# Kernel tuning notes

Measured on AMD Instinct MI355X. Metric: run time of the kernel, lower is better.

## Reference

```python
import jax, jax.numpy as jnp
import numpy as np

EPS = 1e-7

def _dubbed_squash(v):
    norm = jnp.linalg.norm(v, axis=-1, keepdims=True)
    coef = 1.0 - 1.0 / (jnp.exp(norm) + EPS)
    return coef * v / (norm + EPS)

def setup_inputs() -> dict:
    key = jax.random.key(0)
    k1, k2, k3 = jax.random.split(key, 3)
    B, N, dp = 16, 1152, 8   # batch, num_primary_caps, dim_primary_caps
    D, dd = 10, 16           # num_digit_caps, dim_digit_caps
    primary_caps = jax.random.normal(k1, (B, N, dp), dtype=jnp.float32)
    W = jax.random.normal(k2, (D, N, dd, dp), dtype=jnp.float32) * 0.05
    B_prior = jax.random.normal(k3, (D, 1, N), dtype=jnp.float32) * 0.05
    return {"primary_caps": primary_caps, "W": W, "B_prior": B_prior}

def reference(primary_caps, W, B_prior):
    dp = primary_caps.shape[-1]
    # votes: U_hat[b,d,n,j] = W[d,n,j,i] @ u[b,n,i]   (replaces the tf.map_fn)
    U_hat = jnp.einsum('dnji,bni->bdnj', W, primary_caps)  # [B,D,N,dd]
    # self-similarity score matrix (as in original: full NxN matmul)
    A = jnp.einsum('bdnj,bdmj->bdnm', U_hat, U_hat) / jnp.sqrt(
        jnp.asarray(dp, dtype=primary_caps.dtype))          # [B,D,N,N]
    A_sum = jnp.sum(A, axis=2, keepdims=True)               # [B,D,1,N]
    C = jax.nn.softmax(A_sum, axis=1)                       # softmax over digit axis
    # weighted combine with learned log-priors: (B+C) @ U_hat -> [B,D,1,dd] -> squeeze
    S = jnp.einsum('bdkn,bdnj->bdj', B_prior[None] + C, U_hat)  # [B,D,dd]
    return _dubbed_squash(S)
```

## Files before the change

kernel.cpp:

```cpp
#include <hip/hip_runtime.h>

constexpr int BN = 16, NN = 1152, DP = 8, ND = 10, DD = 16;
constexpr int NBLK = BN * ND;
constexpr int GG = 64;
constexpr int KPT = NN / GG;
constexpr unsigned MAG1 = 0xC0FFEE01u;
constexpr int SPIN_CAP = 1 << 20;

__device__ __forceinline__ float ld_dev(const float* p) {
    return __hip_atomic_load(p, __ATOMIC_RELAXED, __HIP_MEMORY_SCOPE_AGENT);
}
__device__ __forceinline__ void st_dev(float* p, float v) {
    __hip_atomic_store(p, v, __ATOMIC_RELAXED, __HIP_MEMORY_SCOPE_AGENT);
}

__global__ __launch_bounds__(1024) void caps_one(
    const float* __restrict__ u, const float* __restrict__ W,
    const float* __restrict__ Bp, float* __restrict__ A,
    unsigned* __restrict__ flags, float* __restrict__ out)
{
    __shared__ float ul[NN * DP];
    __shared__ float coeff[NN];
    __shared__ float Tpart[GG][17];
    __shared__ float Tl[16];
    __shared__ float Spart[GG][17];

    const int t = threadIdx.x;
    const int x = blockIdx.x;
    const int i = (x & 7) * 20 + (x >> 3);
    const int b = i & 15, d = i >> 4;
    const int j = t & 15, g = t >> 4;
    constexpr float RS8 = 0.35355339059327373f;

    {
        const float4* src = reinterpret_cast<const float4*>(u + (size_t)b * NN * DP);
        float4* dst4 = reinterpret_cast<float4*>(ul);
        for (int i2 = t; i2 < NN * DP / 4; i2 += 1024) dst4[i2] = src[i2];
    }
    __syncthreads();

    float uh[KPT];
    float tacc = 0.f;
    const float* Wd = W + (size_t)d * NN * DD * DP;
#pragma unroll 6
    for (int k = 0; k < KPT; ++k) {
        const int n = g + GG * k;
        const float4 w0 = *reinterpret_cast<const float4*>(
            Wd + ((size_t)n * DD + j) * DP);
        const float4 w1 = *reinterpret_cast<const float4*>(
            Wd + ((size_t)n * DD + j) * DP + 4);
        const float4 u0 = reinterpret_cast<const float4*>(ul)[n * 2];
        const float4 u1 = reinterpret_cast<const float4*>(ul)[n * 2 + 1];
        const float s = w0.x * u0.x + w0.y * u0.y + w0.z * u0.z + w0.w * u0.w
                      + w1.x * u1.x + w1.y * u1.y + w1.z * u1.z + w1.w * u1.w;
        uh[k] = s;
        tacc += s;
    }

    Tpart[g][j] = tacc;
    __syncthreads();
    if (t < 16) {
        float s = 0.f;
#pragma unroll
        for (int gg = 0; gg < GG; ++gg) s += Tpart[gg][t];
        Tl[t] = s;
    }
    __syncthreads();

    {
        float* Arow = A + (size_t)(b * ND + d) * NN;
        const float Tj = Tl[j];
#pragma unroll
        for (int k = 0; k < KPT; ++k) {
            float v = Tj * uh[k];
            v += __shfl_xor(v, 8, 16);
            v += __shfl_xor(v, 4, 16);
            v += __shfl_xor(v, 2, 16);
            v += __shfl_xor(v, 1, 16);
            if (j == 0) st_dev(Arow + (g + GG * k), v * RS8);
        }
    }

    __syncthreads();
    if (t == 0)
        __hip_atomic_store(&flags[b * ND + d], MAG1, __ATOMIC_RELAXED,
                           __HIP_MEMORY_SCOPE_AGENT);
    if (t < ND) {
        int spins = 0;
        while (__hip_atomic_load(&flags[b * ND + t], __ATOMIC_RELAXED,
                                 __HIP_MEMORY_SCOPE_AGENT) != MAG1) {
            __builtin_amdgcn_s_sleep(2);
            if (++spins > SPIN_CAP) break;
        }
    }
    asm volatile("" ::: "memory");
    __syncthreads();

    {
        const float* Ab = A + (size_t)b * ND * NN;
        for (int n = t; n < NN; n += 1024) {
            float aq[ND];
#pragma unroll
            for (int q = 0; q < ND; ++q) aq[q] = ld_dev(Ab + (size_t)q * NN + n);
            float m = aq[0];
#pragma unroll
            for (int q = 1; q < ND; ++q) m = fmaxf(m, aq[q]);
            float se = 0.f;
#pragma unroll
            for (int q = 0; q < ND; ++q) { aq[q] = expf(aq[q] - m); se += aq[q]; }
            coeff[n] = Bp[(size_t)d * NN + n] + aq[d] / se;
        }
    }
    __syncthreads();

    float sacc = 0.f;
#pragma unroll
    for (int k = 0; k < KPT; ++k) sacc += coeff[g + GG * k] * uh[k];
    Spart[g][j] = sacc;
    __syncthreads();
    if (t < 16) {
        float Sv = 0.f;
#pragma unroll
        for (int gg = 0; gg < GG; ++gg) Sv += Spart[gg][t];
        float n2 = Sv * Sv;
#pragma unroll
        for (int off = 8; off >= 1; off >>= 1) n2 += __shfl_xor(n2, off, 16);
        const float nrm = sqrtf(n2);
        const float coef = 1.f - 1.f / (expf(nrm) + 1e-7f);
        out[((size_t)b * ND + d) * DD + t] = Sv * (coef / (nrm + 1e-7f));
    }
}

extern "C" void kernel_launch(void* const* d_in, const int* in_sizes, int n_in,
                              void* d_out, int out_size, void* d_ws, size_t ws_size,
                              hipStream_t stream) {
    const float* u  = nullptr;
    const float* W  = nullptr;
    const float* Bp = nullptr;
    for (int i = 0; i < n_in; ++i) {
        const int s = in_sizes[i];
        if (s == BN * NN * DP)            u  = (const float*)d_in[i];
        else if (s == ND * NN * DD * DP)  W  = (const float*)d_in[i];
        else if (s == ND * NN)            Bp = (const float*)d_in[i];
    }
    float* out = (float*)d_out;
    char*  wsc = (char*)d_ws;
    float*    A     = (float*)wsc;
    unsigned* flags = (unsigned*)(wsc + (1u << 20));

    caps_one<<<dim3(NBLK), 1024, 0, stream>>>(u, W, Bp, A, flags, out);
}
```

Baseline: 76.43 us.

## Replace per-element atomic A accesses with plain ops plus explicit cache writeback/invalidate

Drops the relaxed agent-scope atomic loads and stores on the score array A and uses plain stores and float2 vector loads instead. Cross-block visibility is kept by issuing an L2 writeback before the flag store and a cache invalidate after spinning on the flags. It also prefetches the B_prior row into shared memory at the start, overlapping it with the u load. The risk is memory-ordering correctness: the invalidate runs only in the polling threads before the barrier, and the inline asm cache instructions are specific to this architecture.

```diff
diff --git a/kernel.cpp b/kernel.cpp
--- a/kernel.cpp
+++ b/kernel.cpp
@@ -7,19 +7,13 @@
 constexpr unsigned MAG1 = 0xC0FFEE01u;
 constexpr int SPIN_CAP = 1 << 20;
 
-__device__ __forceinline__ float ld_dev(const float* p) {
-    return __hip_atomic_load(p, __ATOMIC_RELAXED, __HIP_MEMORY_SCOPE_AGENT);
-}
-__device__ __forceinline__ void st_dev(float* p, float v) {
-    __hip_atomic_store(p, v, __ATOMIC_RELAXED, __HIP_MEMORY_SCOPE_AGENT);
-}
-
 __global__ __launch_bounds__(1024) void caps_one(
     const float* __restrict__ u, const float* __restrict__ W,
     const float* __restrict__ Bp, float* __restrict__ A,
     unsigned* __restrict__ flags, float* __restrict__ out)
 {
     __shared__ float ul[NN * DP];
+    __shared__ float bpl[NN];
     __shared__ float coeff[NN];
     __shared__ float Tpart[GG][17];
     __shared__ float Tl[16];
@@ -36,6 +30,9 @@
         const float4* src = reinterpret_cast<const float4*>(u + (size_t)b * NN * DP);
         float4* dst4 = reinterpret_cast<float4*>(ul);
         for (int i2 = t; i2 < NN * DP / 4; i2 += 1024) dst4[i2] = src[i2];
+        if (t < NN / 4)
+            reinterpret_cast<float4*>(bpl)[t] =
+                reinterpret_cast<const float4*>(Bp + (size_t)d * NN)[t];
     }
     __syncthreads();
 
@@ -77,14 +74,16 @@
             v += __shfl_xor(v, 4, 16);
             v += __shfl_xor(v, 2, 16);
             v += __shfl_xor(v, 1, 16);
-            if (j == 0) st_dev(Arow + (g + GG * k), v * RS8);
+            if (j == 0) Arow[g + GG * k] = v * RS8;
         }
     }
 
     __syncthreads();
-    if (t == 0)
+    if (t == 0) {
+        asm volatile("buffer_wbl2 sc1\n\ts_waitcnt vmcnt(0)" ::: "memory");
         __hip_atomic_store(&flags[b * ND + d], MAG1, __ATOMIC_RELAXED,
                            __HIP_MEMORY_SCOPE_AGENT);
+    }
     if (t < ND) {
         int spins = 0;
         while (__hip_atomic_load(&flags[b * ND + t], __ATOMIC_RELAXED,
@@ -92,23 +91,35 @@
             __builtin_amdgcn_s_sleep(2);
             if (++spins > SPIN_CAP) break;
         }
+        asm volatile("buffer_inv sc0 sc1\n\ts_waitcnt vmcnt(0)" ::: "memory");
     }
     asm volatile("" ::: "memory");
     __syncthreads();
 
     {
         const float* Ab = A + (size_t)b * ND * NN;
-        for (int n = t; n < NN; n += 1024) {
-            float aq[ND];
+        if (t < NN / 2) {
+            const int n0 = 2 * t;
+            float a0[ND], a1[ND];
 #pragma unroll
-            for (int q = 0; q < ND; ++q) aq[q] = ld_dev(Ab + (size_t)q * NN + n);
-            float m = aq[0];
+            for (int q = 0; q < ND; ++q) {
+                const float2 p = *reinterpret_cast<const float2*>(
+                    Ab + (size_t)q * NN + n0);
+                a0[q] = p.x; a1[q] = p.y;
+            }
+            float m0 = a0[0], m1 = a1[0];
 #pragma unroll
-            for (int q = 1; q < ND; ++q) m = fmaxf(m, aq[q]);
-            float se = 0.f;
+            for (int q = 1; q < ND; ++q) {
+                m0 = fmaxf(m0, a0[q]); m1 = fmaxf(m1, a1[q]);
+            }
+            float se0 = 0.f, se1 = 0.f;
 #pragma unroll
-            for (int q = 0; q < ND; ++q) { aq[q] = expf(aq[q] - m); se += aq[q]; }
-            coeff[n] = Bp[(size_t)d * NN + n] + aq[d] / se;
+            for (int q = 0; q < ND; ++q) {
+                a0[q] = expf(a0[q] - m0); se0 += a0[q];
+                a1[q] = expf(a1[q] - m1); se1 += a1[q];
+            }
+            coeff[n0]     = bpl[n0]     + a0[d] / se0;
+            coeff[n0 + 1] = bpl[n0 + 1] + a1[d] / se1;
         }
     }
     __syncthreads();
```

New measurement: 81.09 us. 1.06x slower.
